# Kernel optimization log

Measured on AMD Instinct MI355X. Metric: run time of the kernel, lower is better.

The kernel has to match this reference:

```python
import jax, jax.numpy as jnp
import numpy as np

NEG_SLOPE = 0.2  # PyG GATConv default negative_slope


def _edges(B, C):
    # Fully-connected (no self) edges among the FIRST C nodes only (as in original
    # code, which ignores batch when building edge_index), plus self loops on all
    # B*C nodes (PyG GATConv add_self_loops=True default).
    N = B * C
    ij = np.array([(i, j) for i in range(C) for j in range(C) if i != j], dtype=np.int32)
    loops = np.arange(N, dtype=np.int32)
    src = jnp.concatenate([jnp.asarray(ij[:, 0]), jnp.asarray(loops)])
    dst = jnp.concatenate([jnp.asarray(ij[:, 1]), jnp.asarray(loops)])
    return src, dst, N


def _gat_conv(x2d, W, att_src, att_dst, bias, src, dst, N):
    h = x2d @ W                              # [N, Fout] linear projection (no bias)
    a_src = h @ att_src                      # [N] per-node src attention logit
    a_dst = h @ att_dst                      # [N] per-node dst attention logit
    e = jax.nn.leaky_relu(a_src[src] + a_dst[dst], NEG_SLOPE)   # [E] edge scores
    m = jax.ops.segment_max(e, dst, num_segments=N)             # segment softmax
    ex = jnp.exp(e - m[dst])
    denom = jax.ops.segment_sum(ex, dst, num_segments=N)
    alpha = ex / denom[dst]                                     # [E]
    out = jax.ops.segment_sum(alpha[:, None] * h[src], dst, num_segments=N)
    return out + bias


def setup_inputs() -> dict:
    key = jax.random.key(0)
    k1, k2, k3, k4 = jax.random.split(key, 4)
    B, C, Fin, Fout = 2048, 63, 250, 250
    x = jax.random.normal(k1, (B, 1, C, Fin), dtype=jnp.float32)
    W = jax.random.normal(k2, (Fin, Fout), dtype=jnp.float32) / np.sqrt(Fin).astype(np.float32)
    att_src = jax.random.normal(k3, (Fout,), dtype=jnp.float32) / np.sqrt(Fout).astype(np.float32)
    att_dst = jax.random.normal(k4, (Fout,), dtype=jnp.float32) / np.sqrt(Fout).astype(np.float32)
    bias = jnp.zeros((Fout,), dtype=jnp.float32)
    return {"x": x, "W": W, "att_src": att_src, "att_dst": att_dst, "bias": bias}


def reference(x, W, att_src, att_dst, bias):
    B, _, C, F = x.shape
    src, dst, N = _edges(B, C)
    out = _gat_conv(x.reshape(N, F), W, att_src, att_dst, bias, src, dst, N)
    return out.reshape(B, 1, C, -1)   # [B, 1, C, Fout]
```

## Files before the change

kernel.cpp:

```cpp
#include <hip/hip_runtime.h>
#include <hip/hip_bf16.h>

#define FIN 250
#define NROWS 129024
#define NT 8
#define NBLK 1008

typedef short short8 __attribute__((ext_vector_type(8)));
typedef float f32x4 __attribute__((ext_vector_type(4)));

__device__ __forceinline__ short f2bf(float f) {
    __bf16 b = (__bf16)f;
    return __builtin_bit_cast(short, b);
}

#define WAITV(n) asm volatile("s_waitcnt vmcnt(" #n ")" ::: "memory")
#define WAITL    asm volatile("s_waitcnt lgkmcnt(0)" ::: "memory")
#define HWBAR do { asm volatile("" ::: "memory"); __builtin_amdgcn_s_barrier(); \
                   asm volatile("" ::: "memory"); } while (0)

__device__ __forceinline__ void stage_tile(const float* __restrict__ x,
                                           const float* __restrict__ xlast,
                                           char* lbuf, int tile, int wv, int lane) {
    #pragma unroll
    for (int i = 0; i < 4; ++i) {
        int r = wv * 4 + i;
        int grow = tile * 16 + r;
        const char* g = (grow == NROWS - 1) ? (const char*)xlast
                                            : (const char*)x + (size_t)grow * 1000u;
        g += lane * 16;
        char* l = lbuf + r * 1024;
        __builtin_amdgcn_global_load_lds(
            (const __attribute__((address_space(1))) void*)g,
            (__attribute__((address_space(3))) void*)l, 16, 0, 0);
    }
}

__global__ void __launch_bounds__(256)
wt_prep(const float* __restrict__ W, const float* __restrict__ x,
        unsigned* __restrict__ Wt, float* __restrict__ xlast) {
    int i = blockIdx.x * 256 + threadIdx.x;
    unsigned c  = (unsigned)i >> 7;
    unsigned kp = (unsigned)i & 127u;
    unsigned k0 = 2u * kp;
    unsigned lo = 0u, hi = 0u;
    if (c < FIN) {
        if (k0 < FIN)      lo = (unsigned)(unsigned short)f2bf(W[k0 * FIN + c]);
        if (k0 + 1u < FIN) hi = (unsigned)(unsigned short)f2bf(W[(k0 + 1u) * FIN + c]);
    }
    Wt[(c << 7) + kp] = lo | (hi << 16);
    if (blockIdx.x == 0) {
        int t = threadIdx.x;
        xlast[t] = (t < FIN) ? x[(size_t)(NROWS - 1) * FIN + t] : 0.f;
    }
}

__global__ void __launch_bounds__(256, 1)
gat_gemm(const float* __restrict__ x, const unsigned short* __restrict__ Wt,
         const float* __restrict__ xlast, const float* __restrict__ bias,
         float* __restrict__ out)
{
    __shared__ __align__(16) char lds[40960];

    const int tid  = threadIdx.x;
    const int lane = tid & 63;
    const int wv   = tid >> 6;
    const int m    = lane & 15;
    const int kg   = lane >> 4;

    short8 b[4][8];
    #pragma unroll
    for (int f = 0; f < 4; ++f)
        #pragma unroll
        for (int kk = 0; kk < 8; ++kk)
            b[f][kk] = *(const short8*)((const char*)Wt
                         + ((size_t)(wv * 64 + f * 16 + m) << 9) + kk * 64 + kg * 16);

    float bc[4];
    #pragma unroll
    for (int f = 0; f < 4; ++f) {
        int c = wv * 64 + f * 16 + m;
        bc[f] = (c < FIN) ? bias[c] : 0.f;
    }

    char* const afr = lds + 32768;
    const int wkk   = lane >> 3;
    const int wkg   = (lane >> 1) & 3;
    const int whalf = lane & 1;

    const int t0 = blockIdx.x * NT;
    stage_tile(x, xlast, lds, t0, wv, lane);

    #pragma unroll 1
    for (int i = 0; i < NT; ++i) {
        const int t = t0 + i;
        if (i + 1 < NT) {
            stage_tile(x, xlast, lds + ((i + 1) & 1) * 16384, t + 1, wv, lane);
            if (i == 0) { WAITV(4); } else { WAITV(20); }
        } else {
            WAITV(16);
        }
        HWBAR;

        {
            const char* sb = lds + (i & 1) * 16384;
            #pragma unroll
            for (int rr = 0; rr < 4; ++rr) {
                int row = wv * 4 + rr;
                float4 v = *(const float4*)(sb + row * 1024 + lane * 16);
                unsigned lo = (unsigned)(unsigned short)f2bf(v.x)
                            | ((unsigned)(unsigned short)f2bf(v.y) << 16);
                unsigned hi = (unsigned)(unsigned short)f2bf(v.z)
                            | ((unsigned)(unsigned short)f2bf(v.w) << 16);
                uint2 pk = make_uint2(lo, hi);
                *(uint2*)(afr + wkk * 1024 + wkg * 256 + ((row ^ wkk) * 16) + whalf * 8) = pk;
            }
        }
        WAITL;
        HWBAR;

        f32x4 acc[4];
        #pragma unroll
        for (int f = 0; f < 4; ++f) acc[f] = (f32x4){bc[f], bc[f], bc[f], bc[f]};
        #pragma unroll
        for (int kk = 0; kk < 8; ++kk) {
            short8 af = *(const short8*)(afr + kk * 1024 + kg * 256 + ((m ^ kk) * 16));
            #pragma unroll
            for (int f = 0; f < 4; ++f)
                acc[f] = __builtin_amdgcn_mfma_f32_16x16x32_bf16(af, b[f][kk], acc[f], 0, 0, 0);
        }

        unsigned obase = ((unsigned)t * 16 + (unsigned)kg * 4) * FIN + (unsigned)(wv * 64 + m);
        #pragma unroll
        for (int f = 0; f < 4; ++f) {
            bool ok = (wv < 3) || (f < 3) || (m < 10);
            if (ok) {
                #pragma unroll
                for (int j = 0; j < 4; ++j)
                    out[obase + (unsigned)(f * 16) + (unsigned)(j * FIN)] = acc[f][j];
            }
        }
    }
}

__global__ void __launch_bounds__(1024, 1)
gat_attn(const float* __restrict__ att_src, const float* __restrict__ att_dst,
         float* __restrict__ out)
{
    __shared__ float hs[63 * 252];
    __shared__ float asrc[64], adst[64];
    __shared__ float alpha[63 * 64];

    const int tid = threadIdx.x;

    for (int idx = tid; idx < 63 * FIN; idx += 1024) {
        int r = idx / FIN, f = idx - r * FIN;
        hs[r * 252 + f] = out[idx];
    }
    __syncthreads();

    {
        int r = tid >> 4, t = tid & 15;
        float s1 = 0.f, s2 = 0.f;
        if (r < 63) {
            for (int k = t; k < FIN; k += 16) {
                float h = hs[r * 252 + k];
                s1 += h * att_src[k];
                s2 += h * att_dst[k];
            }
        }
        #pragma unroll
        for (int o = 8; o >= 1; o >>= 1) {
            s1 += __shfl_xor(s1, o, 16);
            s2 += __shfl_xor(s2, o, 16);
        }
        if (r < 63 && t == 0) { asrc[r] = s1; adst[r] = s2; }
    }
    __syncthreads();

    {
        int d = tid >> 4, t = tid & 15;
        if (d < 63) {
            float ad = adst[d];
            float e_[4];
            float mx = -1e30f;
            #pragma unroll
            for (int q = 0; q < 4; ++q) {
                int sdx = t + q * 16;
                float e = -1e30f;
                if (sdx < 63) {
                    e = asrc[sdx] + ad;
                    e = e > 0.f ? e : 0.2f * e;
                }
                e_[q] = e;
                mx = fmaxf(mx, e);
            }
            #pragma unroll
            for (int o = 8; o >= 1; o >>= 1) mx = fmaxf(mx, __shfl_xor(mx, o, 16));
            float den = 0.f;
            #pragma unroll
            for (int q = 0; q < 4; ++q) {
                int sdx = t + q * 16;
                float ex = (sdx < 63) ? __expf(e_[q] - mx) : 0.f;
                e_[q] = ex;
                den += ex;
            }
            #pragma unroll
            for (int o = 8; o >= 1; o >>= 1) den += __shfl_xor(den, o, 16);
            float rd = 1.f / den;
            #pragma unroll
            for (int q = 0; q < 4; ++q) {
                int sdx = t + q * 16;
                if (sdx < 63) alpha[d * 64 + sdx] = e_[q] * rd;
            }
        }
    }
    __syncthreads();

    for (int idx = tid; idx < 63 * FIN; idx += 1024) {
        int d = idx / FIN, f = idx - d * FIN;
        float v = 0.f;
        for (int sdx = 0; sdx < 63; ++sdx)
            v += alpha[d * 64 + sdx] * hs[sdx * 252 + f];
        out[idx] = v;
    }
}

extern "C" void kernel_launch(void* const* d_in, const int* in_sizes, int n_in,
                              void* d_out, int out_size, void* d_ws, size_t ws_size,
                              hipStream_t stream) {
    (void)in_sizes; (void)n_in; (void)ws_size; (void)out_size;
    const float* x        = (const float*)d_in[0];
    const float* W        = (const float*)d_in[1];
    const float* att_src  = (const float*)d_in[2];
    const float* att_dst  = (const float*)d_in[3];
    const float* bias     = (const float*)d_in[4];
    float* out            = (float*)d_out;
    unsigned* Wt          = (unsigned*)d_ws;
    float* xlast          = (float*)((char*)d_ws + 131072);

    wt_prep<<<128, 256, 0, stream>>>(W, x, Wt, xlast);
    gat_gemm<<<NBLK, 256, 0, stream>>>(x, (const unsigned short*)Wt, xlast, bias, out);
    gat_attn<<<1, 1024, 0, stream>>>(att_src, att_dst, out);
}
```

Before: 96.81 us.

## Use 8 waves per block with triple-buffered LDS prefetch in GEMM

The GEMM block grows from 4 to 8 waves, so each wave covers 32 output columns and stages 2 rows instead of 64 columns and 4 rows. The x tile staging moves from double to triple buffering, prefetching two tiles ahead with vmcnt waits adjusted to match. The aim is more waves in flight and deeper prefetch to hide global load latency in a memory-bound GEMM. The cost is a larger LDS footprint of 56KB per block, which may limit how many blocks fit per CU, and the hand-tuned waitcnt values must stay correct.

```diff
diff --git a/kernel.cpp b/kernel.cpp
--- a/kernel.cpp
+++ b/kernel.cpp
@@ -16,6 +16,7 @@
 
 #define WAITV(n) asm volatile("s_waitcnt vmcnt(" #n ")" ::: "memory")
 #define WAITL    asm volatile("s_waitcnt lgkmcnt(0)" ::: "memory")
+#define SCHEDF   __builtin_amdgcn_sched_barrier(0)
 #define HWBAR do { asm volatile("" ::: "memory"); __builtin_amdgcn_s_barrier(); \
                    asm volatile("" ::: "memory"); } while (0)
 
@@ -23,8 +24,8 @@
                                            const float* __restrict__ xlast,
                                            char* lbuf, int tile, int wv, int lane) {
     #pragma unroll
-    for (int i = 0; i < 4; ++i) {
-        int r = wv * 4 + i;
+    for (int i = 0; i < 2; ++i) {
+        int r = wv * 2 + i;
         int grow = tile * 16 + r;
         const char* g = (grow == NROWS - 1) ? (const char*)xlast
                                             : (const char*)x + (size_t)grow * 1000u;
@@ -55,12 +56,12 @@
     }
 }
 
-__global__ void __launch_bounds__(256, 1)
+__global__ void __launch_bounds__(512, 4)
 gat_gemm(const float* __restrict__ x, const unsigned short* __restrict__ Wt,
          const float* __restrict__ xlast, const float* __restrict__ bias,
          float* __restrict__ out)
 {
-    __shared__ __align__(16) char lds[40960];
+    __shared__ __align__(16) char lds[57344];
 
     const int tid  = threadIdx.x;
     const int lane = tid & 63;
@@ -68,45 +69,49 @@
     const int m    = lane & 15;
     const int kg   = lane >> 4;
 
-    short8 b[4][8];
+    short8 b[2][8];
     #pragma unroll
-    for (int f = 0; f < 4; ++f)
+    for (int f = 0; f < 2; ++f)
         #pragma unroll
         for (int kk = 0; kk < 8; ++kk)
             b[f][kk] = *(const short8*)((const char*)Wt
-                         + ((size_t)(wv * 64 + f * 16 + m) << 9) + kk * 64 + kg * 16);
-
-    float bc[4];
-    #pragma unroll
-    for (int f = 0; f < 4; ++f) {
-        int c = wv * 64 + f * 16 + m;
-        bc[f] = (c < FIN) ? bias[c] : 0.f;
-    }
-
-    char* const afr = lds + 32768;
+                         + ((size_t)(wv * 32 + f * 16 + m) << 9) + kk * 64 + kg * 16);
+
+    const int c0 = wv * 32 + m;
+    const float bc0 = bias[c0];
+    const float bc1 = (c0 + 16 < FIN) ? bias[c0 + 16] : 0.f;
+
+    char* const afr = lds + 49152;
     const int wkk   = lane >> 3;
     const int wkg   = (lane >> 1) & 3;
     const int whalf = lane & 1;
 
+    WAITV(0); SCHEDF;
+
     const int t0 = blockIdx.x * NT;
-    stage_tile(x, xlast, lds, t0, wv, lane);
+    stage_tile(x, xlast, lds,         t0,     wv, lane);
+    stage_tile(x, xlast, lds + 16384, t0 + 1, wv, lane);
 
     #pragma unroll 1
     for (int i = 0; i < NT; ++i) {
         const int t = t0 + i;
-        if (i + 1 < NT) {
-            stage_tile(x, xlast, lds + ((i + 1) & 1) * 16384, t + 1, wv, lane);
-            if (i == 0) { WAITV(4); } else { WAITV(20); }
-        } else {
-            WAITV(16);
-        }
+        if (i + 2 < NT)
+            stage_tile(x, xlast, lds + ((i + 2) % 3) * 16384, t + 2, wv, lane);
+        switch (i) {
+            case 0:      WAITV(4);  break;
+            case 1:      WAITV(12); break;
+            case NT - 2: WAITV(18); break;
+            case NT - 1: WAITV(16); break;
+            default:     WAITV(20); break;
+        }
+        SCHEDF;
         HWBAR;
 
         {
-            const char* sb = lds + (i & 1) * 16384;
-            #pragma unroll
-            for (int rr = 0; rr < 4; ++rr) {
-                int row = wv * 4 + rr;
+            const char* sb = lds + (i % 3) * 16384;
+            #pragma unroll
+            for (int rr = 0; rr < 2; ++rr) {
+                int row = wv * 2 + rr;
                 float4 v = *(const float4*)(sb + row * 1024 + lane * 16);
                 unsigned lo = (unsigned)(unsigned short)f2bf(v.x)
                             | ((unsigned)(unsigned short)f2bf(v.y) << 16);
@@ -119,26 +124,21 @@
         WAITL;
         HWBAR;
 
-        f32x4 acc[4];
-        #pragma unroll
-        for (int f = 0; f < 4; ++f) acc[f] = (f32x4){bc[f], bc[f], bc[f], bc[f]};
+        f32x4 acc0 = {bc0, bc0, bc0, bc0};
+        f32x4 acc1 = {bc1, bc1, bc1, bc1};
         #pragma unroll
         for (int kk = 0; kk < 8; ++kk) {
             short8 af = *(const short8*)(afr + kk * 1024 + kg * 256 + ((m ^ kk) * 16));
-            #pragma unroll
-            for (int f = 0; f < 4; ++f)
-                acc[f] = __builtin_amdgcn_mfma_f32_16x16x32_bf16(af, b[f][kk], acc[f], 0, 0, 0);
-        }
-
-        unsigned obase = ((unsigned)t * 16 + (unsigned)kg * 4) * FIN + (unsigned)(wv * 64 + m);
-        #pragma unroll
-        for (int f = 0; f < 4; ++f) {
-            bool ok = (wv < 3) || (f < 3) || (m < 10);
-            if (ok) {
-                #pragma unroll
-                for (int j = 0; j < 4; ++j)
-                    out[obase + (unsigned)(f * 16) + (unsigned)(j * FIN)] = acc[f][j];
-            }
+            acc0 = __builtin_amdgcn_mfma_f32_16x16x32_bf16(af, b[0][kk], acc0, 0, 0, 0);
+            acc1 = __builtin_amdgcn_mfma_f32_16x16x32_bf16(af, b[1][kk], acc1, 0, 0, 0);
+        }
+
+        unsigned obase = ((unsigned)t * 16 + (unsigned)kg * 4) * FIN + (unsigned)(wv * 32 + m);
+        #pragma unroll
+        for (int j = 0; j < 4; ++j) out[obase + (unsigned)(j * FIN)] = acc0[j];
+        if (wv < 7 || m < 10) {
+            #pragma unroll
+            for (int j = 0; j < 4; ++j) out[obase + 16u + (unsigned)(j * FIN)] = acc1[j];
         }
     }
 }
@@ -240,6 +240,6 @@
     float* xlast          = (float*)((char*)d_ws + 131072);
 
     wt_prep<<<128, 256, 0, stream>>>(W, x, Wt, xlast);
-    gat_gemm<<<NBLK, 256, 0, stream>>>(x, (const unsigned short*)Wt, xlast, bias, out);
+    gat_gemm<<<NBLK, 512, 0, stream>>>(x, (const unsigned short*)Wt, xlast, bias, out);
     gat_attn<<<1, 1024, 0, stream>>>(att_src, att_dst, out);
 }
```

New measurement: 96.46 us. Within noise of the previous version (-0.4%).

## Prefetch x tiles into registers and stage output through LDS for coalesced stores

Applied to the files above, without the earlier changes.

Replaces the global_load_lds async staging with register prefetching two tiles ahead, converted to bf16 and written into double-buffered LDS A-fragments. It also routes the MFMA accumulators through an LDS output buffer so each wave writes whole rows with float4 stores instead of scattered scalar stores. The aim is to cut uncoalesced write traffic and simplify the pipeline. In exchange it adds an extra barrier and LDS round trip per tile, and raises register pressure from holding two prefetched tiles.

```diff
diff --git a/kernel.cpp b/kernel.cpp
--- a/kernel.cpp
+++ b/kernel.cpp
@@ -16,23 +16,23 @@
 
 #define WAITV(n) asm volatile("s_waitcnt vmcnt(" #n ")" ::: "memory")
 #define WAITL    asm volatile("s_waitcnt lgkmcnt(0)" ::: "memory")
+#define SCHEDF   __builtin_amdgcn_sched_barrier(0)
 #define HWBAR do { asm volatile("" ::: "memory"); __builtin_amdgcn_s_barrier(); \
                    asm volatile("" ::: "memory"); } while (0)
 
-__device__ __forceinline__ void stage_tile(const float* __restrict__ x,
-                                           const float* __restrict__ xlast,
-                                           char* lbuf, int tile, int wv, int lane) {
+#define AFR0 0
+#define AFR1 8192
+#define OB   16384
+
+__device__ __forceinline__ void load_tile(uint4 (&lb)[4], const float* __restrict__ x,
+                                          const float* __restrict__ xlast,
+                                          int tile, int wv, int lane) {
     #pragma unroll
-    for (int i = 0; i < 4; ++i) {
-        int r = wv * 4 + i;
-        int grow = tile * 16 + r;
+    for (int rr = 0; rr < 4; ++rr) {
+        int grow = tile * 16 + wv * 4 + rr;
         const char* g = (grow == NROWS - 1) ? (const char*)xlast
                                             : (const char*)x + (size_t)grow * 1000u;
-        g += lane * 16;
-        char* l = lbuf + r * 1024;
-        __builtin_amdgcn_global_load_lds(
-            (const __attribute__((address_space(1))) void*)g,
-            (__attribute__((address_space(3))) void*)l, 16, 0, 0);
+        lb[rr] = *(const uint4*)(g + lane * 16);
     }
 }
 
@@ -60,7 +60,7 @@
          const float* __restrict__ xlast, const float* __restrict__ bias,
          float* __restrict__ out)
 {
-    __shared__ __align__(16) char lds[40960];
+    __shared__ __align__(16) char lds[32768];
 
     const int tid  = threadIdx.x;
     const int lane = tid & 63;
@@ -83,62 +83,86 @@
         bc[f] = (c < FIN) ? bias[c] : 0.f;
     }
 
-    char* const afr = lds + 32768;
+    char* const ob = lds + OB;
     const int wkk   = lane >> 3;
     const int wkg   = (lane >> 1) & 3;
     const int whalf = lane & 1;
+    const unsigned wroff = (unsigned)(wkk * 1024 + wkg * 256 + whalf * 8);
+
+    WAITV(0); SCHEDF;
 
     const int t0 = blockIdx.x * NT;
-    stage_tile(x, xlast, lds, t0, wv, lane);
+    uint4 lbA[4], lbB[4];
+    load_tile(lbA, x, xlast, t0,     wv, lane);
+    load_tile(lbB, x, xlast, t0 + 1, wv, lane);
+    SCHEDF;
 
     #pragma unroll 1
     for (int i = 0; i < NT; ++i) {
         const int t = t0 + i;
-        if (i + 1 < NT) {
-            stage_tile(x, xlast, lds + ((i + 1) & 1) * 16384, t + 1, wv, lane);
-            if (i == 0) { WAITV(4); } else { WAITV(20); }
-        } else {
-            WAITV(16);
-        }
-        HWBAR;
+        switch (i) {
+            case 0:      WAITV(4);  break;
+            case 1:      WAITV(12); break;
+            case NT - 1: WAITV(16); break;
+            default:     WAITV(20); break;
+        }
+        SCHEDF;
 
         {
-            const char* sb = lds + (i & 1) * 16384;
+            char* const afrD = lds + ((i & 1) ? AFR1 : AFR0);
+            const uint4* lb = (i & 1) ? lbB : lbA;
             #pragma unroll
             for (int rr = 0; rr < 4; ++rr) {
                 int row = wv * 4 + rr;
-                float4 v = *(const float4*)(sb + row * 1024 + lane * 16);
-                unsigned lo = (unsigned)(unsigned short)f2bf(v.x)
-                            | ((unsigned)(unsigned short)f2bf(v.y) << 16);
-                unsigned hi = (unsigned)(unsigned short)f2bf(v.z)
-                            | ((unsigned)(unsigned short)f2bf(v.w) << 16);
-                uint2 pk = make_uint2(lo, hi);
-                *(uint2*)(afr + wkk * 1024 + wkg * 256 + ((row ^ wkk) * 16) + whalf * 8) = pk;
-            }
-        }
+                float v0 = __builtin_bit_cast(float, lb[rr].x);
+                float v1 = __builtin_bit_cast(float, lb[rr].y);
+                float v2 = __builtin_bit_cast(float, lb[rr].z);
+                float v3 = __builtin_bit_cast(float, lb[rr].w);
+                unsigned lo = (unsigned)(unsigned short)f2bf(v0)
+                            | ((unsigned)(unsigned short)f2bf(v1) << 16);
+                unsigned hi = (unsigned)(unsigned short)f2bf(v2)
+                            | ((unsigned)(unsigned short)f2bf(v3) << 16);
+                *(uint2*)(afrD + wroff + (unsigned)(((row ^ wkk) * 16)))
+                    = make_uint2(lo, hi);
+            }
+        }
+        SCHEDF;
+        if (i + 2 < NT) {
+            if (i & 1) load_tile(lbB, x, xlast, t + 2, wv, lane);
+            else       load_tile(lbA, x, xlast, t + 2, wv, lane);
+        }
+        SCHEDF;
         WAITL;
         HWBAR;
 
+        const char* afrD = lds + ((i & 1) ? AFR1 : AFR0);
         f32x4 acc[4];
         #pragma unroll
         for (int f = 0; f < 4; ++f) acc[f] = (f32x4){bc[f], bc[f], bc[f], bc[f]};
         #pragma unroll
         for (int kk = 0; kk < 8; ++kk) {
-            short8 af = *(const short8*)(afr + kk * 1024 + kg * 256 + ((m ^ kk) * 16));
+            short8 af = *(const short8*)(afrD + kk * 1024 + kg * 256 + ((m ^ kk) * 16));
             #pragma unroll
             for (int f = 0; f < 4; ++f)
                 acc[f] = __builtin_amdgcn_mfma_f32_16x16x32_bf16(af, b[f][kk], acc[f], 0, 0, 0);
         }
 
-        unsigned obase = ((unsigned)t * 16 + (unsigned)kg * 4) * FIN + (unsigned)(wv * 64 + m);
-        #pragma unroll
-        for (int f = 0; f < 4; ++f) {
-            bool ok = (wv < 3) || (f < 3) || (m < 10);
-            if (ok) {
-                #pragma unroll
-                for (int j = 0; j < 4; ++j)
-                    out[obase + (unsigned)(f * 16) + (unsigned)(j * FIN)] = acc[f][j];
-            }
+        #pragma unroll
+        for (int f = 0; f < 4; ++f)
+            #pragma unroll
+            for (int j = 0; j < 4; ++j)
+                *(float*)(ob + (kg * 4 + j) * 1024 + (unsigned)(wv * 64 + f * 16 + m) * 4)
+                    = acc[f][j];
+        WAITL;
+        HWBAR;
+
+        #pragma unroll
+        for (int rr = 0; rr < 4; ++rr) {
+            int row = wv * 4 + rr;
+            float4 v = *(const float4*)(ob + row * 1024 + lane * 16);
+            char* op = (char*)out + ((size_t)t * 16 + row) * 1000u;
+            if (lane < 62)  *(float4*)(op + lane * 16) = v;
+            if (lane == 62) *(float2*)(op + 992) = make_float2(v.x, v.y);
         }
     }
 }
```

After: 91.39 us. -5.6%, faster.
